# Kernel optimization log

Hardware: AMD Instinct MI355X
Metric: run time of the kernel (lower is better)

Reference implementation:

```python
import jax, jax.numpy as jnp
import numpy as np

D = 256      # x_size
Y = 256      # y_size (c0 / SRU hidden)
H = D // 4   # attention hidden = 64
A = 8        # n_actions


def setup_inputs() -> dict:
    key = jax.random.key(0)
    ks = jax.random.split(key, 10)
    B, L = 32, 2048
    stdv = 1.0 / np.sqrt(H)
    x = jax.random.normal(ks[0], (B, L, D), dtype=jnp.float32)
    c0 = jax.random.normal(ks[1], (B, Y), dtype=jnp.float32)
    x_mask = jnp.zeros((B, L), dtype=bool)
    actions = jax.random.randint(ks[2], (B,), 0, A)
    w1 = jax.random.uniform(ks[3], (A, D, H), minval=-stdv, maxval=stdv, dtype=jnp.float32)
    b1 = jnp.zeros((A, H), dtype=jnp.float32)
    w2 = jax.random.uniform(ks[4], (A, Y, H), minval=-stdv, maxval=stdv, dtype=jnp.float32)
    b2 = jnp.zeros((A, H), dtype=jnp.float32)
    v = jax.random.uniform(ks[5], (A, H), minval=-stdv, maxval=stdv, dtype=jnp.float32)
    # SRU cell weights: input D -> hidden Y, k=3 blocks (x_tilde, f-gate, r-gate)
    w_sru = jax.random.uniform(ks[6], (D, 3 * Y), minval=-stdv, maxval=stdv, dtype=jnp.float32)
    b_sru = jnp.zeros((2 * Y,), dtype=jnp.float32)
    return {"x": x, "x_mask": x_mask, "c0": c0, "actions": actions,
            "w1": w1, "b1": b1, "w2": w2, "b2": b2, "v": v,
            "w_sru": w_sru, "b_sru": b_sru}


def _attention(x, y, x_mask, actions, w1, b1, w2, b2, v):
    # Gather per-batch action params (original does one-hot matmul + expand; same math)
    w1a = w1[actions]            # [B, D, H]
    w2a = w2[actions]            # [B, Y, H]
    b1a = b1[actions]            # [B, H]
    b2a = b2[actions]            # [B, H]
    va = v[actions]              # [B, H]
    x_t = jnp.einsum('bld,bdh->blh', x, w1a) + b1a[:, None, :]
    y_t = jnp.einsum('bd,bdh->bh', y, w2a) + b2a
    inpt = jnp.tanh(x_t + y_t[:, None, :])          # [B, L, H]
    scores = jnp.einsum('blh,bh->bl', inpt, va)      # [B, L]
    return jnp.where(x_mask, -jnp.inf, scores)


def _sru_cell_c(attn_pool, c0, w_sru, b_sru):
    # single-step SRU: c = f * c0 + (1 - f) * x_tilde ; forward()[1] returns c
    u = attn_pool @ w_sru                             # [B, 3Y]
    x_tilde = u[:, :Y]
    f = jax.nn.sigmoid(u[:, Y:2 * Y] + b_sru[:Y])
    return f * c0 + (1.0 - f) * x_tilde


def reference(x, x_mask, c0, actions, w1, b1, w2, b2, v, w_sru, b_sru):
    s_logits = _attention(x, c0, x_mask, actions, w1, b1, w2, b2, v)
    s_probs = jax.nn.softmax(s_logits, axis=-1)
    attn_pool = jnp.einsum('bld,bl->bd', x, s_probs)  # [B, D]
    state = _sru_cell_c(attn_pool, c0, w_sru, b_sru)  # [B, Y]
    e_logits = _attention(x, state, x_mask, actions, w1, b1, w2, b2, v)
    # eval mode: softmax
    return jax.nn.softmax(s_logits, axis=-1), jax.nn.softmax(e_logits, axis=-1)
```

## Files before the change

### kernel.cpp

```cpp
#include <hip/hip_runtime.h>
#include <math.h>

#define B 32
#define L 2048
#define D 256
#define H 64
#define NCHUNK 32
#define LB 64
#define DK 32
#define XS_STRIDE 36

__global__ __launch_bounds__(256) void k2_xt_scores(
    const float* __restrict__ x, const int* __restrict__ actions,
    const float* __restrict__ w1, const float* __restrict__ b1,
    const float* __restrict__ w2, const float* __restrict__ b2,
    const float* __restrict__ c0, const float* __restrict__ v,
    float* __restrict__ xt, float* __restrict__ s_logits,
    float* __restrict__ pool_part, float2* __restrict__ mz) {
  int b  = blockIdx.y;
  int cx = blockIdx.x;
  int l0 = cx * LB;
  int t  = threadIdx.x;
  int th = t & 15;
  int tr = t >> 4;
  int a  = actions[b];
  const float* w1a = w1 + (size_t)a * D * H;
  const float* xb  = x + ((size_t)b * L + l0) * D;

  __shared__ float xs[LB * XS_STRIDE];
  __shared__ float wsd[DK * H];
  __shared__ float red[4][D];
  __shared__ float ys[H];
  __shared__ float slog[LB];
  __shared__ float wrow[LB];

  float* c0s = &red[0][0];
  float* ysp = &red[1][0];

  int xrow0 = t >> 3;          int xcol0 = t & 7;
  int xrow1 = (t + 256) >> 3;  int xcol1 = (t + 256) & 7;
  float4 wpre0 = ((const float4*)w1a)[t];
  float4 wpre1 = ((const float4*)w1a)[t + 256];
  float4 xpre0 = *(const float4*)(xb + (size_t)xrow0 * D + xcol0 * 4);
  float4 xpre1 = *(const float4*)(xb + (size_t)xrow1 * D + xcol1 * 4);

  c0s[t] = c0[b * D + t];
  __syncthreads();
  {
    int h = t & 63;
    int part = t >> 6;
    const float* w = w2 + (size_t)a * D * H;
    float s = 0.0f;
    #pragma unroll 8
    for (int d = part * 64; d < part * 64 + 64; ++d)
      s += c0s[d] * w[d * H + h];
    ysp[part * H + h] = s;
  }
  __syncthreads();
  if (t < H) ys[t] = ysp[t] + ysp[H + t] + ysp[2 * H + t] + ysp[3 * H + t]
                   + b2[a * H + t];

  float acc[4][4];
  #pragma unroll
  for (int i = 0; i < 4; ++i)
    #pragma unroll
    for (int j = 0; j < 4; ++j) acc[i][j] = 0.0f;

  for (int d0 = 0; d0 < D; d0 += DK) {
    __syncthreads();
    ((float4*)wsd)[t]       = wpre0;
    ((float4*)wsd)[t + 256] = wpre1;
    *(float4*)&xs[xrow0 * XS_STRIDE + xcol0 * 4] = xpre0;
    *(float4*)&xs[xrow1 * XS_STRIDE + xcol1 * 4] = xpre1;
    int dn = d0 + DK;
    if (dn < D) {
      const float4* wgn = (const float4*)(w1a + (size_t)dn * H);
      wpre0 = wgn[t];
      wpre1 = wgn[t + 256];
      xpre0 = *(const float4*)(xb + (size_t)xrow0 * D + dn + xcol0 * 4);
      xpre1 = *(const float4*)(xb + (size_t)xrow1 * D + dn + xcol1 * 4);
    }
    __syncthreads();
    #pragma unroll
    for (int dd = 0; dd < DK; dd += 4) {
      float xr[4][4];
      #pragma unroll
      for (int i = 0; i < 4; ++i)
        *(float4*)xr[i] = *(const float4*)&xs[(tr * 4 + i) * XS_STRIDE + dd];
      float wr[4][4];
      #pragma unroll
      for (int k = 0; k < 4; ++k)
        *(float4*)wr[k] = *(const float4*)&wsd[(dd + k) * H + th * 4];
      #pragma unroll
      for (int i = 0; i < 4; ++i)
        #pragma unroll
        for (int k = 0; k < 4; ++k)
          #pragma unroll
          for (int j = 0; j < 4; ++j)
            acc[i][j] += xr[i][k] * wr[k][j];
    }
  }

  float bb[4], vv[4], yy[4];
  #pragma unroll
  for (int j = 0; j < 4; ++j) {
    int h = th * 4 + j;
    bb[j] = b1[a * H + h];
    vv[j] = v[a * H + h];
    yy[j] = ys[h];
  }
  #pragma unroll
  for (int i = 0; i < 4; ++i) {
    int lr = tr * 4 + i;
    int l  = l0 + lr;
    float4 o;
    o.x = acc[i][0] + bb[0];
    o.y = acc[i][1] + bb[1];
    o.z = acc[i][2] + bb[2];
    o.w = acc[i][3] + bb[3];
    *(float4*)(xt + ((size_t)b * L + l) * H + th * 4) = o;
    float p = vv[0] * tanhf(o.x + yy[0]) + vv[1] * tanhf(o.y + yy[1])
            + vv[2] * tanhf(o.z + yy[2]) + vv[3] * tanhf(o.w + yy[3]);
    #pragma unroll
    for (int off = 1; off < 16; off <<= 1) p += __shfl_xor(p, off);
    if (th == 0) {
      s_logits[b * L + l] = p;
      slog[lr] = p;
    }
  }

  __syncthreads();
  if (t < LB) {
    float lv = slog[t];
    float mv = lv;
    #pragma unroll
    for (int off = 1; off < 64; off <<= 1) mv = fmaxf(mv, __shfl_xor(mv, off));
    float wv = expf(lv - mv);
    wrow[t] = wv;
    float zs = wv;
    #pragma unroll
    for (int off = 1; off < 64; off <<= 1) zs += __shfl_xor(zs, off);
    if (t == 0) mz[b * NCHUNK + cx] = make_float2(mv, zs);
  }
  __syncthreads();

  {
    int w    = t >> 6;
    int lane = t & 63;
    const float4* xb4 = (const float4*)xb;
    float4 pacc = make_float4(0.f, 0.f, 0.f, 0.f);
    #pragma unroll 8
    for (int ii = 0; ii < LB / 4; ++ii) {
      int l = w + ii * 4;
      float4 xv = xb4[(size_t)l * 64 + lane];
      float p = wrow[l];
      pacc.x += p * xv.x; pacc.y += p * xv.y;
      pacc.z += p * xv.z; pacc.w += p * xv.w;
    }
    __syncthreads();
    *(float4*)&red[w][lane * 4] = pacc;
    __syncthreads();
    float s = red[0][t] + red[1][t] + red[2][t] + red[3][t];
    pool_part[((size_t)cx * B + b) * D + t] = s;
  }
}

__global__ __launch_bounds__(512) void k5_sru(
    const float* __restrict__ pool_part, const float2* __restrict__ mz,
    const float* __restrict__ c0, const float* __restrict__ w_sru,
    const float* __restrict__ b_sru, const int* __restrict__ actions,
    const float* __restrict__ w2, const float* __restrict__ b2,
    float* __restrict__ y_te, float2* __restrict__ mzf) {
  int b = blockIdx.x;
  int t = threadIdx.x;
  __shared__ float st[D];
  __shared__ float us[512];
  __shared__ float pp[2][D];
  __shared__ float yp[8 * H];
  float m = -3.0e38f;
  float2 mzv[NCHUNK];
  #pragma unroll
  for (int c = 0; c < NCHUNK; ++c) {
    mzv[c] = mz[b * NCHUNK + c];
    m = fmaxf(m, mzv[c].x);
  }
  float Z = 0.0f;
  float sc[NCHUNK];
  #pragma unroll
  for (int c = 0; c < NCHUNK; ++c) {
    sc[c] = expf(mzv[c].x - m);
    Z += sc[c] * mzv[c].y;
  }
  float invZ = 1.0f / Z;
  if (t == 0) mzf[b] = make_float2(m, Z);
  {
    int dim  = t & 255;
    int half = t >> 8;
    float pv = 0.0f;
    #pragma unroll
    for (int c = half * 16; c < half * 16 + 16; ++c)
      pv += sc[c] * pool_part[((size_t)c * B + b) * D + dim];
    pp[half][dim] = pv;
  }
  __syncthreads();
  if (t < D) st[t] = (pp[0][t] + pp[1][t]) * invZ;
  __syncthreads();
  float u = 0.0f;
  #pragma unroll 8
  for (int d = 0; d < D; ++d)
    u += st[d] * w_sru[(size_t)d * 768 + t];
  us[t] = u;
  __syncthreads();
  if (t >= 256) {
    int col = t - 256;
    float f = 1.0f / (1.0f + expf(-(u + b_sru[col])));
    float sv = f * c0[b * D + col] + (1.0f - f) * us[col];
    st[col] = sv;
  }
  __syncthreads();
  int a = actions[b];
  {
    int h = t & 63;
    int part = t >> 6;
    const float* wv = w2 + (size_t)a * D * H;
    float s = 0.0f;
    #pragma unroll 8
    for (int d = part * 32; d < part * 32 + 32; ++d)
      s += st[d] * wv[d * H + h];
    yp[part * H + h] = s;
  }
  __syncthreads();
  if (t < H) {
    float s = 0.0f;
    #pragma unroll
    for (int p = 0; p < 8; ++p) s += yp[p * H + t];
    y_te[b * H + t] = s + b2[a * H + t];
  }
}

__global__ __launch_bounds__(256) void k6_escores(
    const float* __restrict__ xt, const float* __restrict__ y_te,
    const float* __restrict__ v, const int* __restrict__ actions,
    const float* __restrict__ s_logits, const float2* __restrict__ mzf,
    float* __restrict__ e_logits, float* __restrict__ out0) {
  int b    = blockIdx.y;
  int t    = threadIdx.x;
  int w    = t >> 6;
  int lane = t & 63;
  int th   = lane & 15;
  int rg   = lane >> 4;
  int base = blockIdx.x * 64 + w * 16;
  int a    = actions[b];
  float4 yy = *(const float4*)(y_te + b * H + th * 4);
  float4 vv = *(const float4*)(v + a * H + th * 4);
  const float4* xt4 = (const float4*)(xt + (size_t)b * L * H);
  #pragma unroll
  for (int i = 0; i < 4; ++i) {
    int r = base + rg + 4 * i;
    float4 xv = xt4[(size_t)r * 16 + th];
    float p = vv.x * tanhf(xv.x + yy.x) + vv.y * tanhf(xv.y + yy.y)
            + vv.z * tanhf(xv.z + yy.z) + vv.w * tanhf(xv.w + yy.w);
    #pragma unroll
    for (int off = 1; off < 16; off <<= 1) p += __shfl_xor(p, off);
    if (th == 0) e_logits[b * L + r] = p;
  }
  if (t < 64) {
    float2 mzv = mzf[b];
    float invZ = 1.0f / mzv.y;
    int l = blockIdx.x * 64 + t;
    out0[b * L + l] = expf(s_logits[b * L + l] - mzv.x) * invZ;
  }
}

__global__ __launch_bounds__(256) void k_softmax(
    const float* __restrict__ logits, float* __restrict__ out) {
  int b = blockIdx.x;
  int t = threadIdx.x;
  __shared__ float red[4];
  float vals[8];
  float m = -1e30f;
  #pragma unroll
  for (int i = 0; i < 8; ++i) {
    vals[i] = logits[b * L + t + i * 256];
    m = fmaxf(m, vals[i]);
  }
  #pragma unroll
  for (int off = 1; off < 64; off <<= 1) m = fmaxf(m, __shfl_xor(m, off));
  int w = t >> 6;
  if ((t & 63) == 0) red[w] = m;
  __syncthreads();
  m = fmaxf(fmaxf(red[0], red[1]), fmaxf(red[2], red[3]));
  float s = 0.0f;
  #pragma unroll
  for (int i = 0; i < 8; ++i) {
    vals[i] = expf(vals[i] - m);
    s += vals[i];
  }
  #pragma unroll
  for (int off = 1; off < 64; off <<= 1) s += __shfl_xor(s, off);
  __syncthreads();
  if ((t & 63) == 0) red[w] = s;
  __syncthreads();
  s = red[0] + red[1] + red[2] + red[3];
  float inv = 1.0f / s;
  #pragma unroll
  for (int i = 0; i < 8; ++i) out[b * L + t + i * 256] = vals[i] * inv;
}

extern "C" void kernel_launch(void* const* d_in, const int* in_sizes, int n_in,
                              void* d_out, int out_size, void* d_ws, size_t ws_size,
                              hipStream_t stream) {
  const float* x       = (const float*)d_in[0];
  const float* c0      = (const float*)d_in[2];
  const int*   actions = (const int*)d_in[3];
  const float* w1      = (const float*)d_in[4];
  const float* b1      = (const float*)d_in[5];
  const float* w2      = (const float*)d_in[6];
  const float* b2      = (const float*)d_in[7];
  const float* v       = (const float*)d_in[8];
  const float* w_sru   = (const float*)d_in[9];
  const float* b_sru   = (const float*)d_in[10];
  float* out = (float*)d_out;

  float* ws        = (float*)d_ws;
  float* xt        = ws;
  float* s_logits  = xt + (size_t)B * L * H;
  float* e_logits  = s_logits + B * L;
  float* y_te      = e_logits + B * L;
  float* pool_part = y_te + B * H;
  float2* mz       = (float2*)(pool_part + NCHUNK * B * D);
  float2* mzf      = mz + B * NCHUNK;

  k2_xt_scores<<<dim3(NCHUNK, B), 256, 0, stream>>>(
      x, actions, w1, b1, w2, b2, c0, v, xt, s_logits, pool_part, mz);
  k5_sru<<<B, 512, 0, stream>>>(pool_part, mz, c0, w_sru, b_sru, actions,
                                w2, b2, y_te, mzf);
  k6_escores<<<dim3(L / 64, B), 256, 0, stream>>>(
      xt, y_te, v, actions, s_logits, mzf, e_logits, out);
  k_softmax<<<B, 256, 0, stream>>>(e_logits, out + B * L);
}
```

Baseline: 168.4 us.

## Split e-softmax into chunked partial max/sum and a wide finalize kernel

The e-logits softmax no longer runs as a single 32-block kernel. Each k_e block now computes a per-chunk max and sum-of-exp, and a new k_fin kernel with 8x32 blocks merges the chunk statistics and writes both output softmaxes. The intent is to spread the final softmax across more blocks and fold the s-softmax write into the same pass. Separately, the register prefetch pipeline in k2 is replaced by direct global-to-shared loads each iteration, which lowers register pressure but stops load latency from overlapping with compute.

```diff
diff --git a/kernel.cpp b/kernel.cpp
--- a/kernel.cpp
+++ b/kernel.cpp
@@ -37,13 +37,6 @@
   float* c0s = &red[0][0];
   float* ysp = &red[1][0];
 
-  int xrow0 = t >> 3;          int xcol0 = t & 7;
-  int xrow1 = (t + 256) >> 3;  int xcol1 = (t + 256) & 7;
-  float4 wpre0 = ((const float4*)w1a)[t];
-  float4 wpre1 = ((const float4*)w1a)[t + 256];
-  float4 xpre0 = *(const float4*)(xb + (size_t)xrow0 * D + xcol0 * 4);
-  float4 xpre1 = *(const float4*)(xb + (size_t)xrow1 * D + xcol1 * 4);
-
   c0s[t] = c0[b * D + t];
   __syncthreads();
   {
@@ -68,17 +61,19 @@
 
   for (int d0 = 0; d0 < D; d0 += DK) {
     __syncthreads();
-    ((float4*)wsd)[t]       = wpre0;
-    ((float4*)wsd)[t + 256] = wpre1;
-    *(float4*)&xs[xrow0 * XS_STRIDE + xcol0 * 4] = xpre0;
-    *(float4*)&xs[xrow1 * XS_STRIDE + xcol1 * 4] = xpre1;
-    int dn = d0 + DK;
-    if (dn < D) {
-      const float4* wgn = (const float4*)(w1a + (size_t)dn * H);
-      wpre0 = wgn[t];
-      wpre1 = wgn[t + 256];
-      xpre0 = *(const float4*)(xb + (size_t)xrow0 * D + dn + xcol0 * 4);
-      xpre1 = *(const float4*)(xb + (size_t)xrow1 * D + dn + xcol1 * 4);
+    {
+      const float4* g = (const float4*)(w1a + (size_t)d0 * H);
+      float4* s = (float4*)wsd;
+      s[t] = g[t];
+      s[t + 256] = g[t + 256];
+    }
+    #pragma unroll
+    for (int k = 0; k < 2; ++k) {
+      int f4  = t + k * 256;
+      int row = f4 >> 3;
+      int col = f4 & 7;
+      float4 val = *(const float4*)(xb + (size_t)row * D + d0 + col * 4);
+      *(float4*)&xs[row * XS_STRIDE + col * 4] = val;
     }
     __syncthreads();
     #pragma unroll
@@ -165,7 +160,7 @@
   }
 }
 
-__global__ __launch_bounds__(512) void k5_sru(
+__global__ __launch_bounds__(512) void k_mid(
     const float* __restrict__ pool_part, const float2* __restrict__ mz,
     const float* __restrict__ c0, const float* __restrict__ w_sru,
     const float* __restrict__ b_sru, const int* __restrict__ actions,
@@ -214,8 +209,7 @@
   if (t >= 256) {
     int col = t - 256;
     float f = 1.0f / (1.0f + expf(-(u + b_sru[col])));
-    float sv = f * c0[b * D + col] + (1.0f - f) * us[col];
-    st[col] = sv;
+    st[col] = f * c0[b * D + col] + (1.0f - f) * us[col];
   }
   __syncthreads();
   int a = actions[b];
@@ -238,19 +232,20 @@
   }
 }
 
-__global__ __launch_bounds__(256) void k6_escores(
+__global__ __launch_bounds__(256) void k_e(
     const float* __restrict__ xt, const float* __restrict__ y_te,
     const float* __restrict__ v, const int* __restrict__ actions,
-    const float* __restrict__ s_logits, const float2* __restrict__ mzf,
-    float* __restrict__ e_logits, float* __restrict__ out0) {
+    float* __restrict__ e_logits, float2* __restrict__ mz2) {
   int b    = blockIdx.y;
+  int cx   = blockIdx.x;
   int t    = threadIdx.x;
   int w    = t >> 6;
   int lane = t & 63;
   int th   = lane & 15;
   int rg   = lane >> 4;
-  int base = blockIdx.x * 64 + w * 16;
+  int base = cx * 64 + w * 16;
   int a    = actions[b];
+  __shared__ float slog[64];
   float4 yy = *(const float4*)(y_te + b * H + th * 4);
   float4 vv = *(const float4*)(v + a * H + th * 4);
   const float4* xt4 = (const float4*)(xt + (size_t)b * L * H);
@@ -262,49 +257,45 @@
             + vv.z * tanhf(xv.z + yy.z) + vv.w * tanhf(xv.w + yy.w);
     #pragma unroll
     for (int off = 1; off < 16; off <<= 1) p += __shfl_xor(p, off);
-    if (th == 0) e_logits[b * L + r] = p;
-  }
+    if (th == 0) {
+      e_logits[b * L + r] = p;
+      slog[w * 16 + rg + 4 * i] = p;
+    }
+  }
+  __syncthreads();
   if (t < 64) {
-    float2 mzv = mzf[b];
-    float invZ = 1.0f / mzv.y;
-    int l = blockIdx.x * 64 + t;
-    out0[b * L + l] = expf(s_logits[b * L + l] - mzv.x) * invZ;
-  }
-}
-
-__global__ __launch_bounds__(256) void k_softmax(
-    const float* __restrict__ logits, float* __restrict__ out) {
-  int b = blockIdx.x;
+    float lv = slog[t];
+    float mv = lv;
+    #pragma unroll
+    for (int off = 1; off < 64; off <<= 1) mv = fmaxf(mv, __shfl_xor(mv, off));
+    float zs = expf(lv - mv);
+    #pragma unroll
+    for (int off = 1; off < 64; off <<= 1) zs += __shfl_xor(zs, off);
+    if (t == 0) mz2[b * 32 + cx] = make_float2(mv, zs);
+  }
+}
+
+__global__ __launch_bounds__(256) void k_fin(
+    const float* __restrict__ s_logits, const float* __restrict__ e_logits,
+    const float2* __restrict__ mzf, const float2* __restrict__ mz2,
+    float* __restrict__ out0, float* __restrict__ out1) {
+  int b = blockIdx.y;
   int t = threadIdx.x;
-  __shared__ float red[4];
-  float vals[8];
-  float m = -1e30f;
-  #pragma unroll
-  for (int i = 0; i < 8; ++i) {
-    vals[i] = logits[b * L + t + i * 256];
-    m = fmaxf(m, vals[i]);
-  }
-  #pragma unroll
-  for (int off = 1; off < 64; off <<= 1) m = fmaxf(m, __shfl_xor(m, off));
-  int w = t >> 6;
-  if ((t & 63) == 0) red[w] = m;
-  __syncthreads();
-  m = fmaxf(fmaxf(red[0], red[1]), fmaxf(red[2], red[3]));
-  float s = 0.0f;
-  #pragma unroll
-  for (int i = 0; i < 8; ++i) {
-    vals[i] = expf(vals[i] - m);
-    s += vals[i];
-  }
-  #pragma unroll
-  for (int off = 1; off < 64; off <<= 1) s += __shfl_xor(s, off);
-  __syncthreads();
-  if ((t & 63) == 0) red[w] = s;
-  __syncthreads();
-  s = red[0] + red[1] + red[2] + red[3];
-  float inv = 1.0f / s;
-  #pragma unroll
-  for (int i = 0; i < 8; ++i) out[b * L + t + i * 256] = vals[i] * inv;
+  int l = blockIdx.x * 256 + t;
+  float2 vals[32];
+  float m2 = -3.0e38f;
+  #pragma unroll
+  for (int c = 0; c < 32; ++c) {
+    vals[c] = mz2[b * 32 + c];
+    m2 = fmaxf(m2, vals[c].x);
+  }
+  float Z2 = 0.0f;
+  #pragma unroll
+  for (int c = 0; c < 32; ++c)
+    Z2 += expf(vals[c].x - m2) * vals[c].y;
+  float2 ms = mzf[b];
+  out0[b * L + l] = expf(s_logits[b * L + l] - ms.x) / ms.y;
+  out1[b * L + l] = expf(e_logits[b * L + l] - m2) / Z2;
 }
 
 extern "C" void kernel_launch(void* const* d_in, const int* in_sizes, int n_in,
@@ -330,12 +321,13 @@
   float* pool_part = y_te + B * H;
   float2* mz       = (float2*)(pool_part + NCHUNK * B * D);
   float2* mzf      = mz + B * NCHUNK;
+  float2* mz2      = mzf + B;
 
   k2_xt_scores<<<dim3(NCHUNK, B), 256, 0, stream>>>(
       x, actions, w1, b1, w2, b2, c0, v, xt, s_logits, pool_part, mz);
-  k5_sru<<<B, 512, 0, stream>>>(pool_part, mz, c0, w_sru, b_sru, actions,
-                                w2, b2, y_te, mzf);
-  k6_escores<<<dim3(L / 64, B), 256, 0, stream>>>(
-      xt, y_te, v, actions, s_logits, mzf, e_logits, out);
-  k_softmax<<<B, 256, 0, stream>>>(e_logits, out + B * L);
-}
+  k_mid<<<B, 512, 0, stream>>>(pool_part, mz, c0, w_sru, b_sru, actions,
+                               w2, b2, y_te, mzf);
+  k_e<<<dim3(32, B), 256, 0, stream>>>(xt, y_te, v, actions, e_logits, mz2);
+  k_fin<<<dim3(8, B), 256, 0, stream>>>(s_logits, e_logits, mzf, mz2,
+                                        out, out + B * L);
+}
```

Result: no change. 170.6 us (+1.3%).
